# Optimization experiments

Hardware: AMD Instinct MI355X
Metric: run time of the kernel (lower is better)

Reference implementation:

```python
import jax, jax.numpy as jnp
import numpy as np

# Concrete segmented-polynomial instance (uniform 1d):
N = 8192      # nodes (rows of input 0 and of the indexed output)
E = 16384     # edges (batch dim of input 1 and of the per-edge product)
S = 16        # segments per operand (buffer_num_segments, same for all 3 operands)
EXT = 64      # operand_extent (uniform segment shape)
P = 2048      # num_paths of the single operation


def setup_inputs() -> dict:
    key = jax.random.key(0)
    k0, k1, k2, k3, k4, k5 = jax.random.split(key, 6)
    x = jax.random.normal(k0, (N, S * EXT), dtype=jnp.float32)          # node features
    y = jax.random.normal(k1, (E, S * EXT), dtype=jnp.float32)          # edge features
    idx_in = jax.random.randint(k2, (E,), 0, N, dtype=jnp.int32)        # gather index for input 0
    idx_out = jax.random.randint(k3, (E,), 0, N, dtype=jnp.int32)       # scatter index for output 0
    path_indices = jax.random.randint(k4, (P, 3), 0, S, dtype=jnp.int32)  # (i_x, j_y, k_out) per path
    path_coefficients = jax.random.normal(k5, (P,), dtype=jnp.float32)
    return {
        "x": x, "y": y,
        "idx_in": idx_in, "idx_out": idx_out,
        "path_indices": path_indices,
        "path_coefficients": path_coefficients,
    }


def reference(x, y, idx_in, idx_out, path_indices, path_coefficients):
    # Dense path-coefficient tensor C[k, i, j]: duplicate paths accumulate,
    # missing (k,i,j) triples are zero. This is the math-dtype (fp32) contraction
    # the uniform-1d kernel performs over segments of equal extent.
    C = jnp.zeros((S, S, S), dtype=x.dtype).at[
        path_indices[:, 2], path_indices[:, 0], path_indices[:, 1]
    ].add(path_coefficients)

    xr = x.reshape(N, S, EXT)[idx_in]   # gather (BATCH_DIM_INDEXED input): [E, S, EXT]
    yr = y.reshape(E, S, EXT)           # batched input:                    [E, S, EXT]

    # out_e[e, k, c] = sum_{i,j} C[k,i,j] * xr[e,i,c] * yr[e,j,c]
    out_e = jnp.einsum('kij,eic,ejc->ekc', C, xr, yr)

    # scatter-add (BATCH_DIM_INDEXED output) into N output rows
    out = jnp.zeros((N, S, EXT), dtype=x.dtype).at[idx_out].add(out_e)
    return out.reshape(N, S * EXT)
```

## Files before the change

kernel.cpp:

```cpp
#include <hip/hip_runtime.h>
#include <hip/hip_bf16.h>

#define N_NODES 8192
#define E_EDGES 16384
#define S_SEG   16
#define EXT     64
#define P_PATHS 2048
#define ROW     1024
#define L_SLOTS 8
#define NGROUPS (E_EDGES / L_SLOTS)
#define NWAVES  (NGROUPS * 2)
#define NBLK    (NWAVES / 4)

typedef _Float16 f16x8  __attribute__((ext_vector_type(8)));
typedef _Float16 f16x4  __attribute__((ext_vector_type(4)));
typedef _Float16 half2v __attribute__((ext_vector_type(2)));
typedef float    f32x4  __attribute__((ext_vector_type(4)));

#define WS_CMAT  0
#define WS_HIST  8192
#define WS_CURS  40960
#define WS_ROWS  73728
#define WS_ELIST 106512
#define WS_XRS   172048
#define WS_NDS   237584

__global__ void prep(const int* __restrict__ pidx, const float* __restrict__ pcoef,
                     _Float16* __restrict__ Cmat, int* __restrict__ hist) {
    const int tid = threadIdx.x;
    if (blockIdx.x < 32) { hist[blockIdx.x * 256 + tid] = 0; return; }
    __shared__ float sC[S_SEG * S_SEG * S_SEG];
    for (int i = tid; i < 4096; i += 256) sC[i] = 0.f;
    __syncthreads();
    for (int p = tid; p < P_PATHS; p += 256) {
        int i = pidx[3 * p + 0];
        int j = pidx[3 * p + 1];
        int k = pidx[3 * p + 2];
        atomicAdd(&sC[(k * S_SEG + i) * S_SEG + j], pcoef[p]);
    }
    __syncthreads();
    for (int i = tid; i < 4096; i += 256) Cmat[i] = (_Float16)sC[i];
}

__global__ void hist_k(const int* __restrict__ idx_out, int* __restrict__ hist) {
    const int e = blockIdx.x * 256 + threadIdx.x;
    atomicAdd(&hist[idx_out[e]], 1);
}

__global__ __launch_bounds__(256) void scan_k(const int* __restrict__ hist,
                                              int* __restrict__ rows,
                                              int* __restrict__ cursor) {
    __shared__ int part[256];
    const int t = threadIdx.x;
    const int base = t * 32;
    int loc[32];
    int s = 0;
#pragma unroll
    for (int i = 0; i < 32; ++i) { loc[i] = s; s += hist[base + i]; }
    part[t] = s;
    __syncthreads();
    for (int off = 1; off < 256; off <<= 1) {
        int v = part[t];
        int u = (t >= off) ? part[t - off] : 0;
        __syncthreads();
        part[t] = v + u;
        __syncthreads();
    }
    const int excl = (t == 0) ? 0 : part[t - 1];
#pragma unroll
    for (int i = 0; i < 32; ++i) {
        int v = excl + loc[i];
        rows[base + i] = v;
        cursor[base + i] = v;
    }
    if (t == 255) rows[N_NODES] = part[255];
}

__global__ __launch_bounds__(256) void scatter_zero_k(
        const int* __restrict__ idx_in, const int* __restrict__ idx_out,
        int* __restrict__ cursor, int* __restrict__ elist,
        int* __restrict__ xrs, int* __restrict__ nds,
        const int* __restrict__ rows, float* __restrict__ out) {
    const int b = blockIdx.x;
    if (b < E_EDGES / 256) {
        const int e = b * 256 + threadIdx.x;
        const int nd = idx_out[e];
        const int pos = atomicAdd(&cursor[nd], 1);
        elist[pos] = e;
        xrs[pos]   = idx_in[e];
        nds[pos]   = nd;
    } else {
        const int n = (b - E_EDGES / 256) * 4 + (threadIdx.x >> 6);
        const int lane = threadIdx.x & 63;
        const int beg = rows[n], end = rows[n + 1];
        const bool need = (beg == end) || ((beg / L_SLOTS) != ((end - 1) / L_SLOTS));
        if (!need) return;
        const float4 z = {0.f, 0.f, 0.f, 0.f};
        float* ob = out + (size_t)n * ROW + lane * 4;
#pragma unroll
        for (int r = 0; r < 4; ++r) *(float4*)(ob + r * 256) = z;
    }
}

__global__ __launch_bounds__(256, 4) void seg_poly_slots(
        const float* __restrict__ x, const float* __restrict__ y,
        const _Float16* __restrict__ Cmat,
        const int* __restrict__ elist, const int* __restrict__ xrs,
        const int* __restrict__ nds, float* __restrict__ out) {
    __shared__ __attribute__((aligned(16))) _Float16 sx_all[4][S_SEG * 32];
    __shared__ __attribute__((aligned(16))) half2v   sy_all[4][8 * 32];

    const int tid  = threadIdx.x;
    const int lane = tid & 63;
    const int wv   = tid >> 6;
    _Float16* sxh = sx_all[wv];
    half2v*   syp = sy_all[wv];

    const int wid = blockIdx.x * 4 + wv;
    const int g   = wid >> 1;
    const int h   = wid & 1;
    const int s0  = g * L_SLOTS;
    const int c0  = h * 32;

    const int quad = lane >> 4;
    const int m    = lane & 15;
    const int jb2  = (quad & 1) * 4;
    const int ih   = quad >> 1;
    const int jp   = lane >> 3;
    const int c4   = (lane & 7) * 4;

    int e_[L_SLOTS], xr_[L_SLOTS], nd_[L_SLOTS];
    {
        int4 a = *(const int4*)(elist + s0); int4 b = *(const int4*)(elist + s0 + 4);
        e_[0]=a.x; e_[1]=a.y; e_[2]=a.z; e_[3]=a.w; e_[4]=b.x; e_[5]=b.y; e_[6]=b.z; e_[7]=b.w;
        a = *(const int4*)(xrs + s0); b = *(const int4*)(xrs + s0 + 4);
        xr_[0]=a.x; xr_[1]=a.y; xr_[2]=a.z; xr_[3]=a.w; xr_[4]=b.x; xr_[5]=b.y; xr_[6]=b.z; xr_[7]=b.w;
        a = *(const int4*)(nds + s0); b = *(const int4*)(nds + s0 + 4);
        nd_[0]=a.x; nd_[1]=a.y; nd_[2]=a.z; nd_[3]=a.w; nd_[4]=b.x; nd_[5]=b.y; nd_[6]=b.z; nd_[7]=b.w;
    }
    const bool prev_same = (s0 > 0)                  && (nds[s0 - 1]       == nd_[0]);
    const bool next_same = (s0 + L_SLOTS < E_EDGES)  && (nds[s0 + L_SLOTS] == nd_[L_SLOTS - 1]);

    f16x8 afrag[8];
    {
        const _Float16* basep = Cmat + m * 256 + quad * 8;
#pragma unroll
        for (int kk = 0; kk < 8; ++kk) afrag[kk] = *(const f16x8*)(basep + kk * 32);
    }

    float4 xbuf[2][2], ybuf[2][2];
    auto issue = [&](int t, int b) {
        const float* xp = x + (size_t)xr_[t] * ROW + c0;
        const float* yp = y + (size_t)e_[t] * ROW + c0;
        xbuf[b][0] = *(const float4*)(xp + jp * EXT + c4);
        xbuf[b][1] = *(const float4*)(xp + (jp + 8) * EXT + c4);
        ybuf[b][0] = *(const float4*)(yp + (2 * jp)     * EXT + c4);
        ybuf[b][1] = *(const float4*)(yp + (2 * jp + 1) * EXT + c4);
    };
    issue(0, 0);
    issue(1, 1);

    f32x4 acc[2];
#pragma unroll
    for (int ct = 0; ct < 2; ++ct) acc[ct] = f32x4{0.f, 0.f, 0.f, 0.f};
    int segStart = 0;

#pragma unroll
    for (int t = 0; t < L_SLOTS; ++t) {
        const int b = t & 1;

        {
            const float4 v0 = xbuf[b][0], v1 = xbuf[b][1];
            *(f16x4*)(sxh + jp * 32 + c4) =
                f16x4{(_Float16)v0.x, (_Float16)v0.y, (_Float16)v0.z, (_Float16)v0.w};
            *(f16x4*)(sxh + (jp + 8) * 32 + c4) =
                f16x4{(_Float16)v1.x, (_Float16)v1.y, (_Float16)v1.z, (_Float16)v1.w};
            const float4 a0 = ybuf[b][0], a1 = ybuf[b][1];
            *(f16x8*)(syp + jp * 32 + c4) =
                f16x8{(_Float16)a0.x, (_Float16)a1.x, (_Float16)a0.y, (_Float16)a1.y,
                      (_Float16)a0.z, (_Float16)a1.z, (_Float16)a0.w, (_Float16)a1.w};
        }
        if (t + 2 < L_SLOTS) issue(t + 2, b);

#pragma unroll
        for (int ct = 0; ct < 2; ++ct) {
            const int cl = ct * 16 + m;
            half2v ypk[4];
#pragma unroll
            for (int r = 0; r < 4; ++r) ypk[r] = syp[(jb2 + r) * 32 + cl];
#pragma unroll
            for (int kk = 0; kk < 8; ++kk) {
                const _Float16 xh = sxh[(2 * kk + ih) * 32 + cl];
                const half2v hx = {xh, xh};
                const half2v b0 = hx * ypk[0];
                const half2v b1 = hx * ypk[1];
                const half2v b2 = hx * ypk[2];
                const half2v b3 = hx * ypk[3];
                const f16x8 bfrag = {b0[0], b0[1], b1[0], b1[1],
                                     b2[0], b2[1], b3[0], b3[1]};
                acc[ct] = __builtin_amdgcn_mfma_f32_16x16x32_f16(
                              afrag[kk], bfrag, acc[ct], 0, 0, 0);
            }
        }

        const bool last = (t == L_SLOTS - 1);
        if (last || nd_[t + 1] != nd_[t]) {
            const bool shared = (segStart == 0 && prev_same) || (last && next_same);
            float* ob = out + (size_t)nd_[t] * ROW + c0;
            if (shared) {
#pragma unroll
                for (int ct = 0; ct < 2; ++ct)
#pragma unroll
                    for (int r = 0; r < 4; ++r)
                        atomicAdd(ob + (quad * 4 + r) * EXT + ct * 16 + m, acc[ct][r]);
            } else {
#pragma unroll
                for (int ct = 0; ct < 2; ++ct)
#pragma unroll
                    for (int r = 0; r < 4; ++r)
                        ob[(quad * 4 + r) * EXT + ct * 16 + m] = acc[ct][r];
            }
#pragma unroll
            for (int ct = 0; ct < 2; ++ct) acc[ct] = f32x4{0.f, 0.f, 0.f, 0.f};
            segStart = t + 1;
        }
    }
}

extern "C" void kernel_launch(void* const* d_in, const int* in_sizes, int n_in,
                              void* d_out, int out_size, void* d_ws, size_t ws_size,
                              hipStream_t stream) {
    const float* x       = (const float*)d_in[0];
    const float* y       = (const float*)d_in[1];
    const int*   idx_in  = (const int*)d_in[2];
    const int*   idx_out = (const int*)d_in[3];
    const int*   pidx    = (const int*)d_in[4];
    const float* pcoef   = (const float*)d_in[5];
    float* out           = (float*)d_out;

    char* ws = (char*)d_ws;
    _Float16* Cmat = (_Float16*)(ws + WS_CMAT);
    int* hist      = (int*)(ws + WS_HIST);
    int* cursor    = (int*)(ws + WS_CURS);
    int* rows      = (int*)(ws + WS_ROWS);
    int* elist     = (int*)(ws + WS_ELIST);
    int* xrs       = (int*)(ws + WS_XRS);
    int* nds       = (int*)(ws + WS_NDS);

    prep<<<33, 256, 0, stream>>>(pidx, pcoef, Cmat, hist);
    hist_k<<<E_EDGES / 256, 256, 0, stream>>>(idx_out, hist);
    scan_k<<<1, 256, 0, stream>>>(hist, rows, cursor);
    scatter_zero_k<<<E_EDGES / 256 + N_NODES / 4, 256, 0, stream>>>(
        idx_in, idx_out, cursor, elist, xrs, nds, rows, out);
    seg_poly_slots<<<NBLK, 256, 0, stream>>>(x, y, Cmat, elist, xrs, nds, out);
}
```

Baseline: 159.7 us.

## Split into per-edge product pass and sorted per-node reduction pass

Adds a two-phase path. The first kernel computes each edge's output in fp16 with MFMA and writes it to a workspace slot ordered by destination node. The second kernel sums each node's contiguous slice into fp32 output without atomics, and also writes zeros for nodes with no edges, so the separate zeroing step is gone. It removes the slot-grouped scatter accumulation, at the cost of a 32MB fp16 intermediate round trip through memory and fp16 rounding of per-edge results. The path only runs when the workspace is large enough; otherwise the old pipeline is kept.

```diff
diff --git a/kernel.cpp b/kernel.cpp
--- a/kernel.cpp
+++ b/kernel.cpp
@@ -24,6 +24,8 @@
 #define WS_ELIST 106512
 #define WS_XRS   172048
 #define WS_NDS   237584
+#define WS_OUTE  262144
+#define OUTE_BYTES ((size_t)E_EDGES * 1024 * 2)
 
 __global__ void prep(const int* __restrict__ pidx, const float* __restrict__ pcoef,
                      _Float16* __restrict__ Cmat, int* __restrict__ hist) {
@@ -74,6 +76,140 @@
         cursor[base + i] = v;
     }
     if (t == 255) rows[N_NODES] = part[255];
+}
+
+__global__ __launch_bounds__(256) void scatter_pose_k(
+        const int* __restrict__ idx_out, int* __restrict__ cursor,
+        int* __restrict__ pose) {
+    const int e = blockIdx.x * 256 + threadIdx.x;
+    const int nd = idx_out[e];
+    pose[e] = atomicAdd(&cursor[nd], 1);
+}
+
+__global__ __launch_bounds__(256) void p1_edge(
+        const float* __restrict__ x, const float* __restrict__ y,
+        const _Float16* __restrict__ Cmat,
+        const int* __restrict__ idx_in, const int* __restrict__ pose,
+        _Float16* __restrict__ oute) {
+    __shared__ __attribute__((aligned(16))) _Float16 sx_all[4][ROW];
+    __shared__ __attribute__((aligned(16))) half2v   sy_all[4][512];
+
+    const int tid  = threadIdx.x;
+    const int lane = tid & 63;
+    const int wv   = tid >> 6;
+    _Float16* sxh = sx_all[wv];
+    half2v*   syp = sy_all[wv];
+
+    const int e   = blockIdx.x * 4 + wv;
+    const int xr  = idx_in[e];
+    const int pos = pose[e];
+
+    const int quad = lane >> 4;
+    const int m    = lane & 15;
+    const int jb2  = (quad & 1) * 4;
+    const int ih   = quad >> 1;
+    const int jp   = lane >> 3;
+    const int cq   = (lane & 7) * 8;
+
+    f16x8 afrag[8];
+    {
+        const _Float16* basep = Cmat + m * 256 + quad * 8;
+#pragma unroll
+        for (int kk = 0; kk < 8; ++kk) afrag[kk] = *(const f16x8*)(basep + kk * 32);
+    }
+
+    const float* xp = x + (size_t)xr * ROW;
+    const float* yp = y + (size_t)e  * ROW;
+    float4 xb[4], yb[4];
+#pragma unroll
+    for (int k4 = 0; k4 < 4; ++k4)
+        xb[k4] = *(const float4*)(xp + k4 * 256 + lane * 4);
+    yb[0] = *(const float4*)(yp + (2 * jp)     * EXT + cq);
+    yb[1] = *(const float4*)(yp + (2 * jp)     * EXT + cq + 4);
+    yb[2] = *(const float4*)(yp + (2 * jp + 1) * EXT + cq);
+    yb[3] = *(const float4*)(yp + (2 * jp + 1) * EXT + cq + 4);
+
+#pragma unroll
+    for (int k4 = 0; k4 < 4; ++k4) {
+        const float4 v = xb[k4];
+        *(f16x4*)(sxh + k4 * 256 + lane * 4) =
+            f16x4{(_Float16)v.x, (_Float16)v.y, (_Float16)v.z, (_Float16)v.w};
+    }
+    {
+        const float4 a0 = yb[0], a1 = yb[1];
+        const float4 c0 = yb[2], c1 = yb[3];
+        *(f16x8*)(syp + jp * 64 + cq) =
+            f16x8{(_Float16)a0.x, (_Float16)c0.x, (_Float16)a0.y, (_Float16)c0.y,
+                  (_Float16)a0.z, (_Float16)c0.z, (_Float16)a0.w, (_Float16)c0.w};
+        *(f16x8*)(syp + jp * 64 + cq + 4) =
+            f16x8{(_Float16)a1.x, (_Float16)c1.x, (_Float16)a1.y, (_Float16)c1.y,
+                  (_Float16)a1.z, (_Float16)c1.z, (_Float16)a1.w, (_Float16)c1.w};
+    }
+
+    f32x4 acc[4];
+#pragma unroll
+    for (int ct = 0; ct < 4; ++ct) acc[ct] = f32x4{0.f, 0.f, 0.f, 0.f};
+
+#pragma unroll
+    for (int ct = 0; ct < 4; ++ct) {
+        const int c = ct * 16 + m;
+        half2v ypk[4];
+#pragma unroll
+        for (int r = 0; r < 4; ++r) ypk[r] = syp[(jb2 + r) * 64 + c];
+#pragma unroll
+        for (int kk = 0; kk < 8; ++kk) {
+            const _Float16 xh = sxh[(2 * kk + ih) * EXT + c];
+            const half2v hx = {xh, xh};
+            const half2v b0 = hx * ypk[0];
+            const half2v b1 = hx * ypk[1];
+            const half2v b2 = hx * ypk[2];
+            const half2v b3 = hx * ypk[3];
+            const f16x8 bfrag = {b0[0], b0[1], b1[0], b1[1],
+                                 b2[0], b2[1], b3[0], b3[1]};
+            acc[ct] = __builtin_amdgcn_mfma_f32_16x16x32_f16(
+                          afrag[kk], bfrag, acc[ct], 0, 0, 0);
+        }
+    }
+
+#pragma unroll
+    for (int ct = 0; ct < 4; ++ct)
+#pragma unroll
+        for (int r = 0; r < 4; ++r)
+            sxh[(quad * 4 + r) * EXT + ct * 16 + m] = (_Float16)acc[ct][r];
+
+    _Float16* op = oute + (size_t)pos * 1024;
+    *(f16x8*)(op + lane * 8)       = *(const f16x8*)(sxh + lane * 8);
+    *(f16x8*)(op + 512 + lane * 8) = *(const f16x8*)(sxh + 512 + lane * 8);
+}
+
+__global__ __launch_bounds__(256) void p2_reduce(
+        const _Float16* __restrict__ oute, const int* __restrict__ rows,
+        float* __restrict__ out) {
+    const int tid  = threadIdx.x;
+    const int lane = tid & 63;
+    const int wv   = tid >> 6;
+    const int n    = blockIdx.x * 4 + wv;
+    const int beg = rows[n], end = rows[n + 1];
+
+    f32x4 acc[4];
+#pragma unroll
+    for (int q = 0; q < 4; ++q) acc[q] = f32x4{0.f, 0.f, 0.f, 0.f};
+
+    for (int s = beg; s < end; ++s) {
+        const _Float16* bp = oute + (size_t)s * 1024;
+#pragma unroll
+        for (int q = 0; q < 4; ++q) {
+            const f16x4 h = *(const f16x4*)(bp + q * 256 + lane * 4);
+            acc[q][0] += (float)h[0];
+            acc[q][1] += (float)h[1];
+            acc[q][2] += (float)h[2];
+            acc[q][3] += (float)h[3];
+        }
+    }
+    float* ob = out + (size_t)n * ROW;
+#pragma unroll
+    for (int q = 0; q < 4; ++q)
+        *(f32x4*)(ob + q * 256 + lane * 4) = acc[q];
 }
 
 __global__ __launch_bounds__(256) void scatter_zero_k(
@@ -168,7 +304,6 @@
 #pragma unroll
     for (int t = 0; t < L_SLOTS; ++t) {
         const int b = t & 1;
-
         {
             const float4 v0 = xbuf[b][0], v1 = xbuf[b][1];
             *(f16x4*)(sxh + jp * 32 + c4) =
@@ -243,14 +378,25 @@
     int* hist      = (int*)(ws + WS_HIST);
     int* cursor    = (int*)(ws + WS_CURS);
     int* rows      = (int*)(ws + WS_ROWS);
-    int* elist     = (int*)(ws + WS_ELIST);
-    int* xrs       = (int*)(ws + WS_XRS);
-    int* nds       = (int*)(ws + WS_NDS);
-
-    prep<<<33, 256, 0, stream>>>(pidx, pcoef, Cmat, hist);
-    hist_k<<<E_EDGES / 256, 256, 0, stream>>>(idx_out, hist);
-    scan_k<<<1, 256, 0, stream>>>(hist, rows, cursor);
-    scatter_zero_k<<<E_EDGES / 256 + N_NODES / 4, 256, 0, stream>>>(
-        idx_in, idx_out, cursor, elist, xrs, nds, rows, out);
-    seg_poly_slots<<<NBLK, 256, 0, stream>>>(x, y, Cmat, elist, xrs, nds, out);
-}
+
+    if (ws_size >= WS_OUTE + OUTE_BYTES) {
+        int* pose       = (int*)(ws + WS_ELIST);
+        _Float16* oute  = (_Float16*)(ws + WS_OUTE);
+        prep<<<33, 256, 0, stream>>>(pidx, pcoef, Cmat, hist);
+        hist_k<<<E_EDGES / 256, 256, 0, stream>>>(idx_out, hist);
+        scan_k<<<1, 256, 0, stream>>>(hist, rows, cursor);
+        scatter_pose_k<<<E_EDGES / 256, 256, 0, stream>>>(idx_out, cursor, pose);
+        p1_edge<<<E_EDGES / 4, 256, 0, stream>>>(x, y, Cmat, idx_in, pose, oute);
+        p2_reduce<<<N_NODES / 4, 256, 0, stream>>>(oute, rows, out);
+    } else {
+        int* elist     = (int*)(ws + WS_ELIST);
+        int* xrs       = (int*)(ws + WS_XRS);
+        int* nds       = (int*)(ws + WS_NDS);
+        prep<<<33, 256, 0, stream>>>(pidx, pcoef, Cmat, hist);
+        hist_k<<<E_EDGES / 256, 256, 0, stream>>>(idx_out, hist);
+        scan_k<<<1, 256, 0, stream>>>(hist, rows, cursor);
+        scatter_zero_k<<<E_EDGES / 256 + N_NODES / 4, 256, 0, stream>>>(
+            idx_in, idx_out, cursor, elist, xrs, nds, rows, out);
+        seg_poly_slots<<<NBLK, 256, 0, stream>>>(x, y, Cmat, elist, xrs, nds, out);
+    }
+}
```

New measurement: 166.7 us. +4.4%, slower.

## Fuse prep, histogram, scan and scatter into one block; deepen load prefetch

Applied to the files above, without the earlier changes.

Merges the coefficient-tensor build, histogram, prefix scan and counting-sort scatter into a single 1024-thread block that works in LDS. This removes three kernel launches and the global-memory atomics on the histogram, leaving the zero-fill as its own kernel. The main kernel's x/y prefetch grows from two to four slots, raising register pressure, and exclusive output rows are now written with nontemporal stores. The single-block sort serialises 16K edges onto one CU, which may cost more than the launch overhead it removes.

```diff
diff --git a/kernel.cpp b/kernel.cpp
--- a/kernel.cpp
+++ b/kernel.cpp
@@ -1,5 +1,4 @@
 #include <hip/hip_runtime.h>
-#include <hip/hip_bf16.h>
 
 #define N_NODES 8192
 #define E_EDGES 16384
@@ -18,88 +17,94 @@
 typedef float    f32x4  __attribute__((ext_vector_type(4)));
 
 #define WS_CMAT  0
-#define WS_HIST  8192
-#define WS_CURS  40960
 #define WS_ROWS  73728
 #define WS_ELIST 106512
 #define WS_XRS   172048
 #define WS_NDS   237584
 
-__global__ void prep(const int* __restrict__ pidx, const float* __restrict__ pcoef,
-                     _Float16* __restrict__ Cmat, int* __restrict__ hist) {
-    const int tid = threadIdx.x;
-    if (blockIdx.x < 32) { hist[blockIdx.x * 256 + tid] = 0; return; }
+__global__ __launch_bounds__(1024) void prep_sort(
+        const int* __restrict__ pidx, const float* __restrict__ pcoef,
+        const int* __restrict__ idx_in, const int* __restrict__ idx_out,
+        _Float16* __restrict__ Cmat, int* __restrict__ rows,
+        int* __restrict__ elist, int* __restrict__ xrs, int* __restrict__ nds) {
     __shared__ float sC[S_SEG * S_SEG * S_SEG];
-    for (int i = tid; i < 4096; i += 256) sC[i] = 0.f;
-    __syncthreads();
-    for (int p = tid; p < P_PATHS; p += 256) {
-        int i = pidx[3 * p + 0];
-        int j = pidx[3 * p + 1];
-        int k = pidx[3 * p + 2];
-        atomicAdd(&sC[(k * S_SEG + i) * S_SEG + j], pcoef[p]);
-    }
-    __syncthreads();
-    for (int i = tid; i < 4096; i += 256) Cmat[i] = (_Float16)sC[i];
-}
-
-__global__ void hist_k(const int* __restrict__ idx_out, int* __restrict__ hist) {
-    const int e = blockIdx.x * 256 + threadIdx.x;
-    atomicAdd(&hist[idx_out[e]], 1);
-}
-
-__global__ __launch_bounds__(256) void scan_k(const int* __restrict__ hist,
-                                              int* __restrict__ rows,
-                                              int* __restrict__ cursor) {
-    __shared__ int part[256];
+    __shared__ int   histc[N_NODES];
+    __shared__ int   part[1024];
     const int t = threadIdx.x;
-    const int base = t * 32;
-    int loc[32];
-    int s = 0;
-#pragma unroll
-    for (int i = 0; i < 32; ++i) { loc[i] = s; s += hist[base + i]; }
-    part[t] = s;
-    __syncthreads();
-    for (int off = 1; off < 256; off <<= 1) {
-        int v = part[t];
-        int u = (t >= off) ? part[t - off] : 0;
+
+#pragma unroll
+    for (int i = 0; i < 4; ++i) sC[t + i * 1024] = 0.f;
+#pragma unroll
+    for (int i = 0; i < 8; ++i) histc[t + i * 1024] = 0;
+    __syncthreads();
+
+#pragma unroll
+    for (int i = 0; i < 2; ++i) {
+        const int p = t + i * 1024;
+        const int ii = pidx[3 * p + 0];
+        const int jj = pidx[3 * p + 1];
+        const int kk = pidx[3 * p + 2];
+        atomicAdd(&sC[(kk * S_SEG + ii) * S_SEG + jj], pcoef[p]);
+    }
+#pragma unroll
+    for (int i = 0; i < 16; ++i)
+        atomicAdd(&histc[idx_out[t + i * 1024]], 1);
+    __syncthreads();
+
+    {
+        const float* cp = sC + t * 4;
+        *(f16x4*)(Cmat + t * 4) =
+            f16x4{(_Float16)cp[0], (_Float16)cp[1], (_Float16)cp[2], (_Float16)cp[3]};
+    }
+
+    int loc[8];
+    {
+        int s = 0;
+#pragma unroll
+        for (int i = 0; i < 8; ++i) { loc[i] = s; s += histc[t * 8 + i]; }
+        part[t] = s;
+    }
+    __syncthreads();
+    for (int off = 1; off < 1024; off <<= 1) {
+        const int v = part[t];
+        const int u = (t >= off) ? part[t - off] : 0;
         __syncthreads();
         part[t] = v + u;
         __syncthreads();
     }
     const int excl = (t == 0) ? 0 : part[t - 1];
-#pragma unroll
-    for (int i = 0; i < 32; ++i) {
-        int v = excl + loc[i];
-        rows[base + i] = v;
-        cursor[base + i] = v;
-    }
-    if (t == 255) rows[N_NODES] = part[255];
-}
-
-__global__ __launch_bounds__(256) void scatter_zero_k(
-        const int* __restrict__ idx_in, const int* __restrict__ idx_out,
-        int* __restrict__ cursor, int* __restrict__ elist,
-        int* __restrict__ xrs, int* __restrict__ nds,
-        const int* __restrict__ rows, float* __restrict__ out) {
-    const int b = blockIdx.x;
-    if (b < E_EDGES / 256) {
-        const int e = b * 256 + threadIdx.x;
+    __syncthreads();
+#pragma unroll
+    for (int i = 0; i < 8; ++i) {
+        const int v = excl + loc[i];
+        rows[t * 8 + i]  = v;
+        histc[t * 8 + i] = v;
+    }
+    if (t == 1023) rows[N_NODES] = part[1023];
+    __syncthreads();
+
+#pragma unroll
+    for (int i = 0; i < 16; ++i) {
+        const int e  = t + i * 1024;
         const int nd = idx_out[e];
-        const int pos = atomicAdd(&cursor[nd], 1);
+        const int pos = atomicAdd(&histc[nd], 1);
         elist[pos] = e;
         xrs[pos]   = idx_in[e];
         nds[pos]   = nd;
-    } else {
-        const int n = (b - E_EDGES / 256) * 4 + (threadIdx.x >> 6);
-        const int lane = threadIdx.x & 63;
-        const int beg = rows[n], end = rows[n + 1];
-        const bool need = (beg == end) || ((beg / L_SLOTS) != ((end - 1) / L_SLOTS));
-        if (!need) return;
-        const float4 z = {0.f, 0.f, 0.f, 0.f};
-        float* ob = out + (size_t)n * ROW + lane * 4;
-#pragma unroll
-        for (int r = 0; r < 4; ++r) *(float4*)(ob + r * 256) = z;
-    }
+    }
+}
+
+__global__ __launch_bounds__(256) void zerofill_k(const int* __restrict__ rows,
+                                                  float* __restrict__ out) {
+    const int n = blockIdx.x * 4 + (threadIdx.x >> 6);
+    const int lane = threadIdx.x & 63;
+    const int beg = rows[n], end = rows[n + 1];
+    const bool need = (beg == end) || ((beg / L_SLOTS) != ((end - 1) / L_SLOTS));
+    if (!need) return;
+    const float4 z = {0.f, 0.f, 0.f, 0.f};
+    float* ob = out + (size_t)n * ROW + lane * 4;
+#pragma unroll
+    for (int r = 0; r < 4; ++r) *(float4*)(ob + r * 256) = z;
 }
 
 __global__ __launch_bounds__(256, 4) void seg_poly_slots(
@@ -148,7 +153,7 @@
         for (int kk = 0; kk < 8; ++kk) afrag[kk] = *(const f16x8*)(basep + kk * 32);
     }
 
-    float4 xbuf[2][2], ybuf[2][2];
+    float4 xbuf[4][2], ybuf[4][2];
     auto issue = [&](int t, int b) {
         const float* xp = x + (size_t)xr_[t] * ROW + c0;
         const float* yp = y + (size_t)e_[t] * ROW + c0;
@@ -159,6 +164,8 @@
     };
     issue(0, 0);
     issue(1, 1);
+    issue(2, 2);
+    issue(3, 3);
 
     f32x4 acc[2];
 #pragma unroll
@@ -167,7 +174,7 @@
 
 #pragma unroll
     for (int t = 0; t < L_SLOTS; ++t) {
-        const int b = t & 1;
+        const int b = t & 3;
 
         {
             const float4 v0 = xbuf[b][0], v1 = xbuf[b][1];
@@ -180,7 +187,7 @@
                 f16x8{(_Float16)a0.x, (_Float16)a1.x, (_Float16)a0.y, (_Float16)a1.y,
                       (_Float16)a0.z, (_Float16)a1.z, (_Float16)a0.w, (_Float16)a1.w};
         }
-        if (t + 2 < L_SLOTS) issue(t + 2, b);
+        if (t + 4 < L_SLOTS) issue(t + 4, b);
 
 #pragma unroll
         for (int ct = 0; ct < 2; ++ct) {
@@ -218,7 +225,8 @@
                 for (int ct = 0; ct < 2; ++ct)
 #pragma unroll
                     for (int r = 0; r < 4; ++r)
-                        ob[(quad * 4 + r) * EXT + ct * 16 + m] = acc[ct][r];
+                        __builtin_nontemporal_store(
+                            acc[ct][r], ob + (quad * 4 + r) * EXT + ct * 16 + m);
             }
 #pragma unroll
             for (int ct = 0; ct < 2; ++ct) acc[ct] = f32x4{0.f, 0.f, 0.f, 0.f};
@@ -240,17 +248,13 @@
 
     char* ws = (char*)d_ws;
     _Float16* Cmat = (_Float16*)(ws + WS_CMAT);
-    int* hist      = (int*)(ws + WS_HIST);
-    int* cursor    = (int*)(ws + WS_CURS);
     int* rows      = (int*)(ws + WS_ROWS);
     int* elist     = (int*)(ws + WS_ELIST);
     int* xrs       = (int*)(ws + WS_XRS);
     int* nds       = (int*)(ws + WS_NDS);
 
-    prep<<<33, 256, 0, stream>>>(pidx, pcoef, Cmat, hist);
-    hist_k<<<E_EDGES / 256, 256, 0, stream>>>(idx_out, hist);
-    scan_k<<<1, 256, 0, stream>>>(hist, rows, cursor);
-    scatter_zero_k<<<E_EDGES / 256 + N_NODES / 4, 256, 0, stream>>>(
-        idx_in, idx_out, cursor, elist, xrs, nds, rows, out);
+    prep_sort<<<1, 1024, 0, stream>>>(pidx, pcoef, idx_in, idx_out,
+                                      Cmat, rows, elist, xrs, nds);
+    zerofill_k<<<N_NODES / 4, 256, 0, stream>>>(rows, out);
     seg_poly_slots<<<NBLK, 256, 0, stream>>>(x, y, Cmat, elist, xrs, nds, out);
 }
```

New measurement: 232.9 us. 45.9% more time.
